# Kernel optimization log

Measured on AMD Instinct MI355X. Metric: run time of the kernel, lower is better.

## Reference

```python
import jax, jax.numpy as jnp
import numpy as np

N_NODES = 100000
N_EDGES = 3200000
D_IN = 256
D_OUT = 256


def setup_inputs() -> dict:
    key = jax.random.key(0)
    k1, k2, k3, k4, k5, k6 = jax.random.split(key, 6)
    stdv = 1.0 / np.sqrt(D_OUT)
    x = jax.random.normal(k1, (N_NODES, D_IN), dtype=jnp.float32)
    adj_vals = jax.random.uniform(k2, (N_EDGES,), dtype=jnp.float32)
    row = jax.random.randint(k3, (N_EDGES,), 0, N_NODES, dtype=jnp.int32)
    col = jax.random.randint(k4, (N_EDGES,), 0, N_NODES, dtype=jnp.int32)
    weight = jax.random.uniform(k5, (D_IN, D_OUT), minval=-stdv, maxval=stdv, dtype=jnp.float32)
    bias = jax.random.uniform(k6, (D_OUT,), minval=-stdv, maxval=stdv, dtype=jnp.float32)
    return {"x": x, "adj_vals": adj_vals, "row": row, "col": col,
            "weight": weight, "bias": bias}


def reference(x, adj_vals, row, col, weight, bias):
    # support = X @ W   [N, out] -- dense GEMM
    support = x @ weight
    # output = spmm(adj, support): gather source rows, scale by edge value,
    # segment-sum into destination rows.
    msgs = adj_vals[:, None] * support[col]          # [E, out]
    out = jax.ops.segment_sum(msgs, row, num_segments=N_NODES)  # [N, out]
    return out + bias
```

## Files before the change

kernel.cpp:

```cpp
#include <hip/hip_runtime.h>

#define N_NODES 100000
#define N_EDGES 3200000
#define D 256
#define SLOTS 48
#define BK 512
#define NBK 196
#define BCAP 24576
#define PA_EDGES 4096
#define PA_BLOCKS 782

#define QSCALE 0.031496063f
#define QINV   31.75f
#define OUTSCALE (QSCALE / 32767.0f)

typedef unsigned short ushort_t;
typedef unsigned int uint_t;
typedef unsigned long long u64_t;
typedef __attribute__((ext_vector_type(8))) short bf16x8;
typedef __attribute__((ext_vector_type(4))) float f32x4;

static __device__ __forceinline__ ushort_t f2bf(float f) {
  unsigned int u = __float_as_uint(f);
  u = u + 0x7fffu + ((u >> 16) & 1u);
  return (ushort_t)(u >> 16);
}

__global__ __launch_bounds__(256) void init_kernel(const float* __restrict__ w,
                                                   ushort_t* __restrict__ wt,
                                                   int* __restrict__ gcur,
                                                   int* __restrict__ ovf_cnt) {
  int b = blockIdx.x;
  int t = threadIdx.x;
  wt[t * D + b] = f2bf(w[b * D + t]);
  if (b == 0) {
    if (t < 256) gcur[t] = 0;
    if (t == 0) *ovf_cnt = 0;
  }
}

__global__ __launch_bounds__(256) void fused_gemm_bucket(
    const float* __restrict__ x, const ushort_t* __restrict__ wt,
    signed char* __restrict__ support,
    const int* __restrict__ row, const int* __restrict__ col,
    const float* __restrict__ vals,
    int* __restrict__ gcur, u64_t* __restrict__ buckets) {
  __shared__ u64_t smem[4608];

  const int b = blockIdx.x;
  const int t = threadIdx.x;

  if (b % 3 == 0) {
    u64_t* staging = smem;
    uint_t* hist   = (uint_t*)(smem + 4096);
    uint_t* cursor = hist + 256;
    uint_t* base   = cursor + 256;
    uint_t* gbase  = base + 256;

    const int p = b / 3;
    const int e0 = p * PA_EDGES;
    int n = N_EDGES - e0;
    if (n > PA_EDGES) n = PA_EDGES;

    hist[t] = 0;
    __syncthreads();

#pragma unroll
    for (int i = 0; i < 4; ++i) {
      int g = i * 256 + t;
      if (g * 4 < n) {
        int4 r = *(const int4*)(row + e0 + g * 4);
        atomicAdd(&hist[r.x >> 9], 1u);
        atomicAdd(&hist[r.y >> 9], 1u);
        atomicAdd(&hist[r.z >> 9], 1u);
        atomicAdd(&hist[r.w >> 9], 1u);
      }
    }
    __syncthreads();

    uint_t v = hist[t];
    base[t] = v;
    __syncthreads();
#pragma unroll
    for (int d = 1; d < 256; d <<= 1) {
      uint_t add = (t >= d) ? base[t - d] : 0;
      __syncthreads();
      base[t] += add;
      __syncthreads();
    }
    uint_t excl = base[t] - v;
    __syncthreads();
    base[t] = excl;
    cursor[t] = excl;
    gbase[t] = (uint_t)atomicAdd(&gcur[t], (int)v);
    __syncthreads();

#pragma unroll
    for (int i = 0; i < 4; ++i) {
      int g = i * 256 + t;
      if (g * 4 < n) {
        int4 r = *(const int4*)(row + e0 + g * 4);
        int4 c = *(const int4*)(col + e0 + g * 4);
        float4 vv = *(const float4*)(vals + e0 + g * 4);
        uint_t q0 = (uint_t)__float2int_rn(vv.x * 32767.f);
        uint_t q1 = (uint_t)__float2int_rn(vv.y * 32767.f);
        uint_t q2 = (uint_t)__float2int_rn(vv.z * 32767.f);
        uint_t q3 = (uint_t)__float2int_rn(vv.w * 32767.f);
        uint_t pos;
        pos = atomicAdd(&cursor[r.x >> 9], 1u);
        staging[pos] = ((u64_t)(uint_t)r.x << 32) | ((q0 << 17) | (uint_t)c.x);
        pos = atomicAdd(&cursor[r.y >> 9], 1u);
        staging[pos] = ((u64_t)(uint_t)r.y << 32) | ((q1 << 17) | (uint_t)c.y);
        pos = atomicAdd(&cursor[r.z >> 9], 1u);
        staging[pos] = ((u64_t)(uint_t)r.z << 32) | ((q2 << 17) | (uint_t)c.z);
        pos = atomicAdd(&cursor[r.w >> 9], 1u);
        staging[pos] = ((u64_t)(uint_t)r.w << 32) | ((q3 << 17) | (uint_t)c.w);
      }
    }
    __syncthreads();

    int ntot = (int)base[255] + (int)hist[255];
    for (int j = t; j < ntot; j += 256) {
      u64_t e = staging[j];
      int bk = (int)(e >> 41);
      uint_t d = gbase[bk] + (uint_t)j - base[bk];
      buckets[(size_t)bk * BCAP + d] = e;
    }
    return;
  }

  ushort_t* A_lds = (ushort_t*)smem;
  ushort_t* B_lds = A_lds + 128 * 40;
  const int gb = (b / 3) * 2 + (b % 3) - 1;
  const int m0 = (gb >> 1) * 128;
  const int n0 = (gb & 1) * 128;
  const int lane = t & 63;
  const int wid = t >> 6;
  const int wm = wid >> 1;
  const int wn = wid & 1;

  f32x4 acc[4][4];
#pragma unroll
  for (int i = 0; i < 4; ++i)
#pragma unroll
    for (int j = 0; j < 4; ++j) acc[i][j] = (f32x4){0.f, 0.f, 0.f, 0.f};

  for (int k0 = 0; k0 < D; k0 += 32) {
#pragma unroll
    for (int p = 0; p < 4; ++p) {
      int f = t + p * 256;
      int r = f >> 3;
      int q = f & 7;
      f32x4 v = (f32x4){0.f, 0.f, 0.f, 0.f};
      if (m0 + r < N_NODES)
        v = __builtin_nontemporal_load(
            (const f32x4*)(x + (size_t)(m0 + r) * D + k0) + q);
      ushort4 o;
      o.x = f2bf(v.x); o.y = f2bf(v.y); o.z = f2bf(v.z); o.w = f2bf(v.w);
      *(ushort4*)&A_lds[r * 40 + q * 4] = o;
    }
#pragma unroll
    for (int p = 0; p < 2; ++p) {
      int f = t + p * 256;
      int r = f >> 2;
      int c = (f & 3) * 8;
      *(uint4*)&B_lds[r * 40 + c] =
          *(const uint4*)(wt + (size_t)(n0 + r) * D + k0 + c);
    }
    __syncthreads();

    bf16x8 aF[4], bF[4];
#pragma unroll
    for (int fm = 0; fm < 4; ++fm)
      aF[fm] = *(const bf16x8*)&A_lds[(wm * 64 + fm * 16 + (lane & 15)) * 40 + (lane >> 4) * 8];
#pragma unroll
    for (int fn = 0; fn < 4; ++fn)
      bF[fn] = *(const bf16x8*)&B_lds[(wn * 64 + fn * 16 + (lane & 15)) * 40 + (lane >> 4) * 8];

#pragma unroll
    for (int fm = 0; fm < 4; ++fm)
#pragma unroll
      for (int fn = 0; fn < 4; ++fn)
        acc[fm][fn] = __builtin_amdgcn_mfma_f32_16x16x32_bf16(
            aF[fm], bF[fn], acc[fm][fn], 0, 0, 0);
    __syncthreads();
  }

#pragma unroll
  for (int fm = 0; fm < 4; ++fm) {
#pragma unroll
    for (int fn = 0; fn < 4; ++fn) {
#pragma unroll
      for (int r = 0; r < 4; ++r) {
        int m = m0 + wm * 64 + fm * 16 + (lane >> 4) * 4 + r;
        int n = n0 + wn * 64 + fn * 16 + (lane & 15);
        if (m < N_NODES) {
          int q = __float2int_rn(acc[fm][fn][r] * QINV);
          q = q > 127 ? 127 : (q < -127 ? -127 : q);
          support[(size_t)m * D + n] = (signed char)q;
        }
      }
    }
  }
}

__global__ __launch_bounds__(1024) void bucket_to_slots(
    const int* __restrict__ gcur, const u64_t* __restrict__ buckets,
    uint_t* __restrict__ slots, int* __restrict__ cnt,
    int* __restrict__ ovf_cnt, u64_t* __restrict__ ovf) {
  __shared__ uint_t slotbuf[BK * SLOTS];
  __shared__ uint_t lcnt[BK];

  const int b = blockIdx.x;
  const int t = threadIdx.x;
  for (int i = t; i < BK; i += 1024) lcnt[i] = 0;
  __syncthreads();

  const int n = gcur[b];
  const u64_t* src = buckets + (size_t)b * BCAP;
  for (int i = t; i < n; i += 1024) {
    u64_t e = src[i];
    int rl = ((int)(e >> 32)) & (BK - 1);
    uint_t k = atomicAdd(&lcnt[rl], 1u);
    if (k < SLOTS) slotbuf[rl * SLOTS + k] = (uint_t)e;
    else ovf[atomicAdd(ovf_cnt, 1)] = e;
  }
  __syncthreads();

  uint_t* dst = slots + (size_t)b * (BK * SLOTS);
  for (int i = t * 4; i < BK * SLOTS; i += 1024 * 4)
    *(uint4*)(dst + i) = *(const uint4*)(slotbuf + i);
  for (int i = t; i < BK; i += 1024) {
    int r = b * BK + i;
    if (r < N_NODES) cnt[r] = (int)lcnt[i];
  }
}

__global__ __launch_bounds__(256) void spmm_kernel(
    const int* __restrict__ cnt, const uint_t* __restrict__ slots,
    const signed char* __restrict__ support, const float* __restrict__ bias,
    float* __restrict__ out) {
  int wid = blockIdx.x * 4 + (threadIdx.x >> 6);
  int lane = threadIdx.x & 63;
  if (wid >= N_NODES) return;

  int n = cnt[wid];
  if (n > SLOTS) n = SLOTS;
  const uint_t* base = slots + (size_t)wid * SLOTS;

  uint_t ed = 0;
  if (lane < n) ed = __builtin_nontemporal_load(base + lane);

  const int quarter = lane >> 4;
  const int sub = lane & 15;

  int a0 = 0, a1 = 0, a2 = 0, a3 = 0, a4 = 0, a5 = 0, a6 = 0, a7 = 0;
  int a8 = 0, a9 = 0, a10 = 0, a11 = 0, a12 = 0, a13 = 0, a14 = 0, a15 = 0;
  int nq = (n + 3) >> 2;
#pragma unroll 2
  for (int i = 0; i < nq; ++i) {
    uint_t u = (uint_t)__shfl((int)ed, 4 * i + quarter);
    int vq = (int)(u >> 17);
    int c = (int)(u & 0x1FFFFu);
    uint4 s = *(const uint4*)(support + (size_t)c * D + sub * 16);
    int sx = (int)s.x, sy = (int)s.y, sz = (int)s.z, sw = (int)s.w;
    a0  += __mul24(vq, (sx << 24) >> 24);
    a1  += __mul24(vq, (sx << 16) >> 24);
    a2  += __mul24(vq, (sx << 8) >> 24);
    a3  += __mul24(vq, sx >> 24);
    a4  += __mul24(vq, (sy << 24) >> 24);
    a5  += __mul24(vq, (sy << 16) >> 24);
    a6  += __mul24(vq, (sy << 8) >> 24);
    a7  += __mul24(vq, sy >> 24);
    a8  += __mul24(vq, (sz << 24) >> 24);
    a9  += __mul24(vq, (sz << 16) >> 24);
    a10 += __mul24(vq, (sz << 8) >> 24);
    a11 += __mul24(vq, sz >> 24);
    a12 += __mul24(vq, (sw << 24) >> 24);
    a13 += __mul24(vq, (sw << 16) >> 24);
    a14 += __mul24(vq, (sw << 8) >> 24);
    a15 += __mul24(vq, sw >> 24);
  }

  a0  += __shfl_xor(a0, 16);  a0  += __shfl_xor(a0, 32);
  a1  += __shfl_xor(a1, 16);  a1  += __shfl_xor(a1, 32);
  a2  += __shfl_xor(a2, 16);  a2  += __shfl_xor(a2, 32);
  a3  += __shfl_xor(a3, 16);  a3  += __shfl_xor(a3, 32);
  a4  += __shfl_xor(a4, 16);  a4  += __shfl_xor(a4, 32);
  a5  += __shfl_xor(a5, 16);  a5  += __shfl_xor(a5, 32);
  a6  += __shfl_xor(a6, 16);  a6  += __shfl_xor(a6, 32);
  a7  += __shfl_xor(a7, 16);  a7  += __shfl_xor(a7, 32);
  a8  += __shfl_xor(a8, 16);  a8  += __shfl_xor(a8, 32);
  a9  += __shfl_xor(a9, 16);  a9  += __shfl_xor(a9, 32);
  a10 += __shfl_xor(a10, 16); a10 += __shfl_xor(a10, 32);
  a11 += __shfl_xor(a11, 16); a11 += __shfl_xor(a11, 32);
  a12 += __shfl_xor(a12, 16); a12 += __shfl_xor(a12, 32);
  a13 += __shfl_xor(a13, 16); a13 += __shfl_xor(a13, 32);
  a14 += __shfl_xor(a14, 16); a14 += __shfl_xor(a14, 32);
  a15 += __shfl_xor(a15, 16); a15 += __shfl_xor(a15, 32);

  int b0 = quarter == 0 ? a0 : quarter == 1 ? a4 : quarter == 2 ? a8 : a12;
  int b1 = quarter == 0 ? a1 : quarter == 1 ? a5 : quarter == 2 ? a9 : a13;
  int b2 = quarter == 0 ? a2 : quarter == 1 ? a6 : quarter == 2 ? a10 : a14;
  int b3 = quarter == 0 ? a3 : quarter == 1 ? a7 : quarter == 2 ? a11 : a15;
  int oidx = sub * 4 + quarter;
  f32x4 bv = ((const f32x4*)bias)[oidx];
  f32x4 o;
  o.x = (float)b0 * OUTSCALE + bv.x;
  o.y = (float)b1 * OUTSCALE + bv.y;
  o.z = (float)b2 * OUTSCALE + bv.z;
  o.w = (float)b3 * OUTSCALE + bv.w;
  __builtin_nontemporal_store(o, (f32x4*)out + (size_t)wid * 64 + oidx);
}

__global__ __launch_bounds__(256) void spill_kernel(
    const int* __restrict__ ovf_cnt, const u64_t* __restrict__ ovf,
    const signed char* __restrict__ support, float* __restrict__ out) {
  int n = *ovf_cnt;
  int w = blockIdx.x * 4 + (threadIdx.x >> 6);
  int lane = threadIdx.x & 63;
  for (int i = w; i < n; i += gridDim.x * 4) {
    u64_t e = ovf[i];
    int r = (int)(e >> 32);
    uint_t u = (uint_t)e;
    int c = (int)(u & 0x1FFFFu);
    float vS = (float)(u >> 17) * OUTSCALE;
    int su = ((const int*)(support + (size_t)c * D))[lane];
    float* o = out + (size_t)r * D + lane * 4;
    atomicAdd(o + 0, vS * (float)((su << 24) >> 24));
    atomicAdd(o + 1, vS * (float)((su << 16) >> 24));
    atomicAdd(o + 2, vS * (float)((su << 8) >> 24));
    atomicAdd(o + 3, vS * (float)(su >> 24));
  }
}

extern "C" void kernel_launch(void* const* d_in, const int* in_sizes, int n_in,
                              void* d_out, int out_size, void* d_ws,
                              size_t ws_size, hipStream_t stream) {
  const float* x    = (const float*)d_in[0];
  const float* vals = (const float*)d_in[1];
  const int* row    = (const int*)d_in[2];
  const int* col    = (const int*)d_in[3];
  const float* w    = (const float*)d_in[4];
  const float* bias = (const float*)d_in[5];
  float* out = (float*)d_out;

  char* p = (char*)d_ws;
  signed char* support = (signed char*)p; p += (size_t)N_NODES * D;
  ushort_t* wt = (ushort_t*)p;       p += (size_t)D * D * 2;
  u64_t* buckets = (u64_t*)p;        p += (size_t)NBK * BCAP * 8;
  uint_t* slots = (uint_t*)p;        p += (size_t)NBK * BK * SLOTS * 4;
  int* cnt = (int*)p;                p += (size_t)N_NODES * 4;
  int* gcur = (int*)p;               p += 1024;
  int* ovf_cnt = (int*)p;            p += 256;
  u64_t* ovf = (u64_t*)p;            p += (size_t)131072 * 8;

  init_kernel<<<256, 256, 0, stream>>>(w, wt, gcur, ovf_cnt);

  fused_gemm_bucket<<<3 * PA_BLOCKS, 256, 0, stream>>>(x, wt, support, row,
                                                       col, vals, gcur,
                                                       buckets);

  bucket_to_slots<<<NBK, 1024, 0, stream>>>(gcur, buckets, slots, cnt,
                                            ovf_cnt, ovf);

  spmm_kernel<<<(N_NODES + 3) / 4, 256, 0, stream>>>(cnt, slots, support,
                                                     bias, out);

  spill_kernel<<<256, 256, 0, stream>>>(ovf_cnt, ovf, support, out);
}
```

Measured before the change: 233.1 us.

## Use finer 128-row buckets and 64-row GEMM tiles with single-pass edge loading

Row buckets shrink from 512 to 128 rows, giving 782 buckets, so bucket_to_slots runs as 782 smaller 256-thread blocks instead of 196 blocks of 1024 threads. The partition blocks now read row/col/vals once, keep the packed entries in registers, and pack global and local bucket bases into one word. GEMM blocks now compute 64 rows by all 256 columns per tile instead of 128x128. This trades more global atomics on gcur and more bucket-base bookkeeping for better load balance and fewer passes over the edge arrays.

```diff
diff --git a/kernel.cpp b/kernel.cpp
--- a/kernel.cpp
+++ b/kernel.cpp
@@ -4,11 +4,12 @@
 #define N_EDGES 3200000
 #define D 256
 #define SLOTS 48
-#define BK 512
-#define NBK 196
-#define BCAP 24576
+#define BK 128
+#define NBK 782
+#define BCAP 5120
 #define PA_EDGES 4096
 #define PA_BLOCKS 782
+#define GB 1564
 
 #define QSCALE 0.031496063f
 #define QINV   31.75f
@@ -33,10 +34,11 @@
   int b = blockIdx.x;
   int t = threadIdx.x;
   wt[t * D + b] = f2bf(w[b * D + t]);
-  if (b == 0) {
-    if (t < 256) gcur[t] = 0;
-    if (t == 0) *ovf_cnt = 0;
-  }
+  if (b < 4) {
+    int g = b * 256 + t;
+    if (g < 1024) gcur[g] = 0;
+  }
+  if (b == 0 && t == 0) *ovf_cnt = 0;
 }
 
 __global__ __launch_bounds__(256) void fused_gemm_bucket(
@@ -45,99 +47,109 @@
     const int* __restrict__ row, const int* __restrict__ col,
     const float* __restrict__ vals,
     int* __restrict__ gcur, u64_t* __restrict__ buckets) {
-  __shared__ u64_t smem[4608];
+  __shared__ u64_t staging[PA_EDGES];
+  __shared__ uint_t histcur[784];
+  __shared__ uint_t scanb[256];
+  __shared__ uint_t bg[784];
 
   const int b = blockIdx.x;
   const int t = threadIdx.x;
 
   if (b % 3 == 0) {
-    u64_t* staging = smem;
-    uint_t* hist   = (uint_t*)(smem + 4096);
-    uint_t* cursor = hist + 256;
-    uint_t* base   = cursor + 256;
-    uint_t* gbase  = base + 256;
-
     const int p = b / 3;
     const int e0 = p * PA_EDGES;
     int n = N_EDGES - e0;
     if (n > PA_EDGES) n = PA_EDGES;
 
-    hist[t] = 0;
-    __syncthreads();
-
-#pragma unroll
-    for (int i = 0; i < 4; ++i) {
-      int g = i * 256 + t;
-      if (g * 4 < n) {
-        int4 r = *(const int4*)(row + e0 + g * 4);
-        atomicAdd(&hist[r.x >> 9], 1u);
-        atomicAdd(&hist[r.y >> 9], 1u);
-        atomicAdd(&hist[r.z >> 9], 1u);
-        atomicAdd(&hist[r.w >> 9], 1u);
+    for (int i = t; i < 784; i += 256) histcur[i] = 0;
+    __syncthreads();
+
+    u64_t ent[16];
+#pragma unroll
+    for (int g = 0; g < 4; ++g) {
+      if (g * 1024 < n) {
+        int e = e0 + g * 1024 + t * 4;
+        int4 r = *(const int4*)(row + e);
+        int4 c = *(const int4*)(col + e);
+        float4 v = *(const float4*)(vals + e);
+        uint_t q0 = (uint_t)__float2int_rn(v.x * 32767.f);
+        uint_t q1 = (uint_t)__float2int_rn(v.y * 32767.f);
+        uint_t q2 = (uint_t)__float2int_rn(v.z * 32767.f);
+        uint_t q3 = (uint_t)__float2int_rn(v.w * 32767.f);
+        ent[g * 4 + 0] = ((u64_t)(uint_t)r.x << 32) | ((q0 << 17) | (uint_t)c.x);
+        ent[g * 4 + 1] = ((u64_t)(uint_t)r.y << 32) | ((q1 << 17) | (uint_t)c.y);
+        ent[g * 4 + 2] = ((u64_t)(uint_t)r.z << 32) | ((q2 << 17) | (uint_t)c.z);
+        ent[g * 4 + 3] = ((u64_t)(uint_t)r.w << 32) | ((q3 << 17) | (uint_t)c.w);
+        atomicAdd(&histcur[r.x >> 7], 1u);
+        atomicAdd(&histcur[r.y >> 7], 1u);
+        atomicAdd(&histcur[r.z >> 7], 1u);
+        atomicAdd(&histcur[r.w >> 7], 1u);
       }
     }
     __syncthreads();
 
-    uint_t v = hist[t];
-    base[t] = v;
+    uint_t h0 = 0, h1 = 0, h2 = 0, h3 = 0;
+    if (t < 196) {
+      h0 = histcur[4 * t];     h1 = histcur[4 * t + 1];
+      h2 = histcur[4 * t + 2]; h3 = histcur[4 * t + 3];
+    }
+    uint_t tot = h0 + h1 + h2 + h3;
+    scanb[t] = tot;
     __syncthreads();
 #pragma unroll
     for (int d = 1; d < 256; d <<= 1) {
-      uint_t add = (t >= d) ? base[t - d] : 0;
+      uint_t add = (t >= d) ? scanb[t - d] : 0;
       __syncthreads();
-      base[t] += add;
+      scanb[t] += add;
       __syncthreads();
     }
-    uint_t excl = base[t] - v;
-    __syncthreads();
-    base[t] = excl;
-    cursor[t] = excl;
-    gbase[t] = (uint_t)atomicAdd(&gcur[t], (int)v);
-    __syncthreads();
-
-#pragma unroll
-    for (int i = 0; i < 4; ++i) {
-      int g = i * 256 + t;
-      if (g * 4 < n) {
-        int4 r = *(const int4*)(row + e0 + g * 4);
-        int4 c = *(const int4*)(col + e0 + g * 4);
-        float4 vv = *(const float4*)(vals + e0 + g * 4);
-        uint_t q0 = (uint_t)__float2int_rn(vv.x * 32767.f);
-        uint_t q1 = (uint_t)__float2int_rn(vv.y * 32767.f);
-        uint_t q2 = (uint_t)__float2int_rn(vv.z * 32767.f);
-        uint_t q3 = (uint_t)__float2int_rn(vv.w * 32767.f);
-        uint_t pos;
-        pos = atomicAdd(&cursor[r.x >> 9], 1u);
-        staging[pos] = ((u64_t)(uint_t)r.x << 32) | ((q0 << 17) | (uint_t)c.x);
-        pos = atomicAdd(&cursor[r.y >> 9], 1u);
-        staging[pos] = ((u64_t)(uint_t)r.y << 32) | ((q1 << 17) | (uint_t)c.y);
-        pos = atomicAdd(&cursor[r.z >> 9], 1u);
-        staging[pos] = ((u64_t)(uint_t)r.z << 32) | ((q2 << 17) | (uint_t)c.z);
-        pos = atomicAdd(&cursor[r.w >> 9], 1u);
-        staging[pos] = ((u64_t)(uint_t)r.w << 32) | ((q3 << 17) | (uint_t)c.w);
+    uint_t excl = scanb[t] - tot;
+    __syncthreads();
+    if (t < 196) {
+      uint_t b0 = excl, b1 = b0 + h0, b2 = b1 + h1, b3 = b2 + h2;
+      uint_t g0 = h0 ? (uint_t)atomicAdd(&gcur[4 * t], (int)h0) : 0u;
+      uint_t g1 = h1 ? (uint_t)atomicAdd(&gcur[4 * t + 1], (int)h1) : 0u;
+      uint_t g2 = h2 ? (uint_t)atomicAdd(&gcur[4 * t + 2], (int)h2) : 0u;
+      uint_t g3 = h3 ? (uint_t)atomicAdd(&gcur[4 * t + 3], (int)h3) : 0u;
+      bg[4 * t]     = (g0 << 16) | b0;
+      bg[4 * t + 1] = (g1 << 16) | b1;
+      bg[4 * t + 2] = (g2 << 16) | b2;
+      bg[4 * t + 3] = (g3 << 16) | b3;
+      histcur[4 * t] = b0;     histcur[4 * t + 1] = b1;
+      histcur[4 * t + 2] = b2; histcur[4 * t + 3] = b3;
+    }
+    __syncthreads();
+
+#pragma unroll
+    for (int g = 0; g < 4; ++g) {
+      if (g * 1024 < n) {
+#pragma unroll
+        for (int j = 0; j < 4; ++j) {
+          u64_t e = ent[g * 4 + j];
+          int bk = (int)(e >> 39);
+          uint_t pos = atomicAdd(&histcur[bk], 1u);
+          staging[pos] = e;
+        }
       }
     }
     __syncthreads();
 
-    int ntot = (int)base[255] + (int)hist[255];
-    for (int j = t; j < ntot; j += 256) {
+    for (int j = t; j < n; j += 256) {
       u64_t e = staging[j];
-      int bk = (int)(e >> 41);
-      uint_t d = gbase[bk] + (uint_t)j - base[bk];
+      int bk = (int)(e >> 39);
+      uint_t u = bg[bk];
+      uint_t d = (u >> 16) + (uint_t)j - (u & 0xFFFFu);
       buckets[(size_t)bk * BCAP + d] = e;
     }
     return;
   }
 
-  ushort_t* A_lds = (ushort_t*)smem;
-  ushort_t* B_lds = A_lds + 128 * 40;
+  ushort_t* A_lds = (ushort_t*)staging;
+  ushort_t* B_lds = A_lds + 64 * 40;
   const int gb = (b / 3) * 2 + (b % 3) - 1;
-  const int m0 = (gb >> 1) * 128;
-  const int n0 = (gb & 1) * 128;
+  const int m0 = gb * 64;
   const int lane = t & 63;
-  const int wid = t >> 6;
-  const int wm = wid >> 1;
-  const int wn = wid & 1;
+  const int wn = t >> 6;
 
   f32x4 acc[4][4];
 #pragma unroll
@@ -147,7 +159,7 @@
 
   for (int k0 = 0; k0 < D; k0 += 32) {
 #pragma unroll
-    for (int p = 0; p < 4; ++p) {
+    for (int p = 0; p < 2; ++p) {
       int f = t + p * 256;
       int r = f >> 3;
       int q = f & 7;
@@ -160,19 +172,19 @@
       *(ushort4*)&A_lds[r * 40 + q * 4] = o;
     }
 #pragma unroll
-    for (int p = 0; p < 2; ++p) {
+    for (int p = 0; p < 4; ++p) {
       int f = t + p * 256;
       int r = f >> 2;
       int c = (f & 3) * 8;
       *(uint4*)&B_lds[r * 40 + c] =
-          *(const uint4*)(wt + (size_t)(n0 + r) * D + k0 + c);
+          *(const uint4*)(wt + (size_t)r * D + k0 + c);
     }
     __syncthreads();
 
     bf16x8 aF[4], bF[4];
 #pragma unroll
     for (int fm = 0; fm < 4; ++fm)
-      aF[fm] = *(const bf16x8*)&A_lds[(wm * 64 + fm * 16 + (lane & 15)) * 40 + (lane >> 4) * 8];
+      aF[fm] = *(const bf16x8*)&A_lds[(fm * 16 + (lane & 15)) * 40 + (lane >> 4) * 8];
 #pragma unroll
     for (int fn = 0; fn < 4; ++fn)
       bF[fn] = *(const bf16x8*)&B_lds[(wn * 64 + fn * 16 + (lane & 15)) * 40 + (lane >> 4) * 8];
@@ -192,8 +204,8 @@
     for (int fn = 0; fn < 4; ++fn) {
 #pragma unroll
       for (int r = 0; r < 4; ++r) {
-        int m = m0 + wm * 64 + fm * 16 + (lane >> 4) * 4 + r;
-        int n = n0 + wn * 64 + fn * 16 + (lane & 15);
+        int m = m0 + fm * 16 + (lane >> 4) * 4 + r;
+        int n = wn * 64 + fn * 16 + (lane & 15);
         if (m < N_NODES) {
           int q = __float2int_rn(acc[fm][fn][r] * QINV);
           q = q > 127 ? 127 : (q < -127 ? -127 : q);
@@ -204,7 +216,7 @@
   }
 }
 
-__global__ __launch_bounds__(1024) void bucket_to_slots(
+__global__ __launch_bounds__(256) void bucket_to_slots(
     const int* __restrict__ gcur, const u64_t* __restrict__ buckets,
     uint_t* __restrict__ slots, int* __restrict__ cnt,
     int* __restrict__ ovf_cnt, u64_t* __restrict__ ovf) {
@@ -213,12 +225,12 @@
 
   const int b = blockIdx.x;
   const int t = threadIdx.x;
-  for (int i = t; i < BK; i += 1024) lcnt[i] = 0;
+  if (t < BK) lcnt[t] = 0;
   __syncthreads();
 
   const int n = gcur[b];
   const u64_t* src = buckets + (size_t)b * BCAP;
-  for (int i = t; i < n; i += 1024) {
+  for (int i = t; i < n; i += 256) {
     u64_t e = src[i];
     int rl = ((int)(e >> 32)) & (BK - 1);
     uint_t k = atomicAdd(&lcnt[rl], 1u);
@@ -228,11 +240,11 @@
   __syncthreads();
 
   uint_t* dst = slots + (size_t)b * (BK * SLOTS);
-  for (int i = t * 4; i < BK * SLOTS; i += 1024 * 4)
+  for (int i = t * 4; i < BK * SLOTS; i += 256 * 4)
     *(uint4*)(dst + i) = *(const uint4*)(slotbuf + i);
-  for (int i = t; i < BK; i += 1024) {
-    int r = b * BK + i;
-    if (r < N_NODES) cnt[r] = (int)lcnt[i];
+  if (t < BK) {
+    int r = b * BK + t;
+    if (r < N_NODES) cnt[r] = (int)lcnt[t];
   }
 }
 
@@ -351,7 +363,7 @@
   u64_t* buckets = (u64_t*)p;        p += (size_t)NBK * BCAP * 8;
   uint_t* slots = (uint_t*)p;        p += (size_t)NBK * BK * SLOTS * 4;
   int* cnt = (int*)p;                p += (size_t)N_NODES * 4;
-  int* gcur = (int*)p;               p += 1024;
+  int* gcur = (int*)p;               p += 4096;
   int* ovf_cnt = (int*)p;            p += 256;
   u64_t* ovf = (u64_t*)p;            p += (size_t)131072 * 8;
 
@@ -361,8 +373,8 @@
                                                        col, vals, gcur,
                                                        buckets);
 
-  bucket_to_slots<<<NBK, 1024, 0, stream>>>(gcur, buckets, slots, cnt,
-                                            ovf_cnt, ovf);
+  bucket_to_slots<<<NBK, 256, 0, stream>>>(gcur, buckets, slots, cnt,
+                                           ovf_cnt, ovf);
 
   spmm_kernel<<<(N_NODES + 3) / 4, 256, 0, stream>>>(cnt, slots, support,
                                                      bias, out);
```

Measured after the change: 234.0 us. Within noise of the previous version (+0.4%).
